# Optimization experiments

Measured on AMD Instinct MI355X. Metric: run time of the kernel, lower is better.

## Reference

```python
import jax, jax.numpy as jnp
import numpy as np

N_EMBD = 1024
N_HEAD = 16
B, T = 4, 2048

def setup_inputs() -> dict:
    key = jax.random.key(0)
    ks = jax.random.split(key, 5)
    s_attn = 1.0 / np.sqrt(N_EMBD)
    s_proj = 1.0 / np.sqrt(N_EMBD)
    return {
        "x": jax.random.normal(ks[0], (B, T, N_EMBD), dtype=jnp.float32),
        "w_attn": jax.random.uniform(ks[1], (N_EMBD, 3 * N_EMBD), jnp.float32, -s_attn, s_attn),
        "b_attn": jax.random.uniform(ks[2], (3 * N_EMBD,), jnp.float32, -s_attn, s_attn),
        "w_proj": jax.random.uniform(ks[3], (N_EMBD, N_EMBD), jnp.float32, -s_proj, s_proj),
        "b_proj": jax.random.uniform(ks[4], (N_EMBD,), jnp.float32, -s_proj, s_proj),
    }

def reference(x, w_attn, b_attn, w_proj, b_proj):
    Bx, Tx, C = x.shape
    hd = C // N_HEAD  # head dim
    qkv = x @ w_attn + b_attn                       # [B,T,3C]
    q, k, v = jnp.split(qkv, 3, axis=-1)
    # [B,T,C] -> [B,H,T,hd]
    def heads(t):
        return t.reshape(Bx, Tx, N_HEAD, hd).transpose(0, 2, 1, 3)
    q, k, v = heads(q), heads(k), heads(v)
    att = jnp.einsum('bhqd,bhkd->bhqk', q, k) * (1.0 / np.sqrt(hd))
    causal = jnp.tril(jnp.ones((Tx, Tx), dtype=bool))
    att = jnp.where(causal, att, -jnp.inf)
    att = jax.nn.softmax(att, axis=-1)
    y = jnp.einsum('bhqk,bhkd->bhqd', att, v)       # [B,H,T,hd]
    y = y.transpose(0, 2, 1, 3).reshape(Bx, Tx, C)
    return y @ w_proj + b_proj
```

## Files before the change

kernel.cpp:

```cpp
#include <hip/hip_runtime.h>
#include <cstdint>

typedef unsigned short u16;
typedef short s16x8 __attribute__((ext_vector_type(8)));
typedef short s16x4 __attribute__((ext_vector_type(4)));
typedef float f32x4 __attribute__((ext_vector_type(4)));

#define B_   4
#define T_   2048
#define C_   1024
#define H_   16
#define HD_  64
#define M_   8192
#define N3_  3072

#define QSCALE 0.18033688011112042f

__device__ inline u16 f2b(float f) {
  union { float f; uint32_t u; } v; v.f = f;
  uint32_t u = v.u;
  return (u16)((u + 0x7FFFu + ((u >> 16) & 1u)) >> 16);
}

__device__ inline f32x4 mfma16(s16x4 a, s16x4 b, f32x4 c) {
#if __has_builtin(__builtin_amdgcn_mfma_f32_16x16x16bf16_1k)
  return __builtin_amdgcn_mfma_f32_16x16x16bf16_1k(a, b, c, 0, 0, 0);
#else
  f32x4 d;
  asm("v_mfma_f32_16x16x16_bf16 %0, %1, %2, %3"
      : "=v"(d) : "v"(a), "v"(b), "v"(c));
  return d;
#endif
}

__device__ inline void gload_lds16(const void* g, void* l) {
  __builtin_amdgcn_global_load_lds(
      (const __attribute__((address_space(1))) void*)g,
      (__attribute__((address_space(3))) void*)l, 16, 0, 0);
}

__global__ __launch_bounds__(256) void cvt_f32_bf16(
    const float* __restrict__ in, u16* __restrict__ out, int n) {
  int i = (blockIdx.x * 256 + threadIdx.x) * 8;
  if (i >= n) return;
  float4 a = *(const float4*)(in + i);
  float4 b = *(const float4*)(in + i + 4);
  s16x8 r;
  r[0] = (short)f2b(a.x); r[1] = (short)f2b(a.y);
  r[2] = (short)f2b(a.z); r[3] = (short)f2b(a.w);
  r[4] = (short)f2b(b.x); r[5] = (short)f2b(b.y);
  r[6] = (short)f2b(b.z); r[7] = (short)f2b(b.w);
  *(s16x8*)(out + i) = r;
}

__global__ __launch_bounds__(256) void cvt_transpose(
    const float* __restrict__ W, u16* __restrict__ WT, int K, int N) {
  __shared__ u16 tile[64][65];
  int n0 = blockIdx.x * 64, k0 = blockIdx.y * 64;
  int j = threadIdx.x & 63, i0 = threadIdx.x >> 6;
#pragma unroll
  for (int i = i0; i < 64; i += 4)
    tile[i][j] = f2b(W[(size_t)(k0 + i) * N + n0 + j]);
  __syncthreads();
#pragma unroll
  for (int i = i0; i < 64; i += 4)
    WT[(size_t)(n0 + i) * K + k0 + j] = tile[j][i];
}

template <int MODE>
__global__ __launch_bounds__(256, 2) void gemm_bt(
    const u16* __restrict__ A, const u16* __restrict__ Bt,
    const float* __restrict__ bias, float* __restrict__ outf,
    u16* __restrict__ qo, u16* __restrict__ ko, u16* __restrict__ vo,
    int M, int N, int K) {
  __shared__ u16 As[128 * 32];
  __shared__ u16 Bs[128 * 32];
  int bid = blockIdx.x;
  int nbn = N >> 7;
  int bm = bid / nbn, bn = bid % nbn;
  int m0 = bm * 128, n0 = bn * 128;
  int tid = threadIdx.x;
  int lane = tid & 63, w = tid >> 6;
  int wm = (w >> 1) * 64, wn = (w & 1) * 64;
  int l15 = lane & 15, g = lane >> 4;

  f32x4 acc[4][4] = {};

  for (int kb = 0; kb < K; kb += 32) {
    __syncthreads();
#pragma unroll
    for (int it = 0; it < 2; ++it) {
      int idx = it * 256 + tid;
      int row = idx >> 2, kc = (idx & 3) * 8;
      gload_lds16(A  + (size_t)(m0 + row) * K + kb + kc, &As[idx * 8]);
      gload_lds16(Bt + (size_t)(n0 + row) * K + kb + kc, &Bs[idx * 8]);
    }
    __syncthreads();

    s16x8 af[4], bf[4];
#pragma unroll
    for (int mi = 0; mi < 4; ++mi)
      af[mi] = *(const s16x8*)&As[(wm + mi * 16 + l15) * 32 + g * 8];
#pragma unroll
    for (int ni = 0; ni < 4; ++ni)
      bf[ni] = *(const s16x8*)&Bs[(wn + ni * 16 + l15) * 32 + g * 8];
#pragma unroll
    for (int mi = 0; mi < 4; ++mi)
#pragma unroll
      for (int ni = 0; ni < 4; ++ni)
        acc[mi][ni] = __builtin_amdgcn_mfma_f32_16x16x32_bf16(
            af[mi], bf[ni], acc[mi][ni], 0, 0, 0);
  }

#pragma unroll
  for (int mi = 0; mi < 4; ++mi)
#pragma unroll
    for (int ni = 0; ni < 4; ++ni) {
      int col = n0 + wn + ni * 16 + l15;
      float bv = bias[col];
#pragma unroll
      for (int r = 0; r < 4; ++r) {
        int row = m0 + wm + mi * 16 + g * 4 + r;
        float val = acc[mi][ni][r] + bv;
        if (MODE == 0) {
          outf[(size_t)row * N + col] = val;
        } else {
          int which = col >> 10, hc = col & 1023;
          int h = hc >> 6, d = hc & 63;
          int b = row >> 11, t = row & 2047;
          if (which == 0) val *= QSCALE;
          u16* dst = (which == 0) ? qo : (which == 1) ? ko : vo;
          dst[(((size_t)(b * 16 + h)) * 2048 + t) * 64 + d] = f2b(val);
        }
      }
    }
}

__global__ __launch_bounds__(256, 2) void attn_fwd(
    const u16* __restrict__ Q, const u16* __restrict__ Kg,
    const u16* __restrict__ V, u16* __restrict__ Y) {
  __shared__ u16 Ks[64 * 72];
  __shared__ u16 Vt[64 * 66];

  int bid = blockIdx.x;
  int bh = bid & 63;
  int qt = 31 - (bid >> 6);
  int tid = threadIdx.x, lane = tid & 63, w = tid >> 6;
  int l15 = lane & 15, g = lane >> 4;

  const u16* Qh = Q  + (size_t)bh * T_ * HD_;
  const u16* Kh = Kg + (size_t)bh * T_ * HD_;
  const u16* Vh = V  + (size_t)bh * T_ * HD_;

  int q0 = qt * 64 + w * 16;
  int qrow = q0 + l15;

  s16x8 qa[2];
#pragma unroll
  for (int ks = 0; ks < 2; ++ks)
    qa[ks] = *(const s16x8*)(Qh + (size_t)qrow * HD_ + g * 8 + ks * 32);

  f32x4 oacc[4] = {};
  float m = -3.0e30f, l = 0.f;

  int vr = tid >> 3, vc = (tid & 7) * 8;
  int kr = tid >> 2, kc = (tid & 3) * 16;

  int ntile = qt + 1;
  for (int kt = 0; kt < ntile; ++kt) {
    int kvb = kt * 64;
    __syncthreads();
    {
      const u16* krow = Kh + (size_t)(kvb + kr) * HD_ + kc;
      *(s16x8*)&Ks[kr * 72 + kc]     = *(const s16x8*)krow;
      *(s16x8*)&Ks[kr * 72 + kc + 8] = *(const s16x8*)(krow + 8);
#pragma unroll
      for (int hh = 0; hh < 2; ++hh) {
        int kv = vr + hh * 32;
        s16x8 vv = *(const s16x8*)(Vh + (size_t)(kvb + kv) * HD_ + vc);
#pragma unroll
        for (int i = 0; i < 8; ++i) Vt[(vc + i) * 66 + kv] = (u16)vv[i];
      }
    }
    __syncthreads();

    f32x4 sacc[4] = {};
#pragma unroll
    for (int cf = 0; cf < 4; ++cf)
#pragma unroll
      for (int ks = 0; ks < 2; ++ks) {
        s16x8 kb = *(const s16x8*)&Ks[(cf * 16 + l15) * 72 + g * 8 + ks * 32];
        sacc[cf] = __builtin_amdgcn_mfma_f32_16x16x32_bf16(kb, qa[ks], sacc[cf], 0, 0, 0);
      }

    if (kt == qt) {
#pragma unroll
      for (int cf = 0; cf < 4; ++cf)
#pragma unroll
        for (int r = 0; r < 4; ++r) {
          int kv = kvb + cf * 16 + g * 4 + r;
          if (kv > qrow) sacc[cf][r] = -1e30f;
        }
    }

    float mx = sacc[0][0];
#pragma unroll
    for (int cf = 0; cf < 4; ++cf)
#pragma unroll
      for (int r = 0; r < 4; ++r) mx = fmaxf(mx, sacc[cf][r]);
    mx = fmaxf(mx, __shfl_xor(mx, 16, 64));
    mx = fmaxf(mx, __shfl_xor(mx, 32, 64));

    float mn = fmaxf(m, mx);
    float alpha = __builtin_amdgcn_exp2f(m - mn);
    m = mn;

    float rs = 0.f;
#pragma unroll
    for (int cf = 0; cf < 4; ++cf)
#pragma unroll
      for (int r = 0; r < 4; ++r) {
        float p = __builtin_amdgcn_exp2f(sacc[cf][r] - mn);
        sacc[cf][r] = p;
        rs += p;
      }
    rs += __shfl_xor(rs, 16, 64);
    rs += __shfl_xor(rs, 32, 64);
    l = l * alpha + rs;
#pragma unroll
    for (int df = 0; df < 4; ++df)
#pragma unroll
      for (int r = 0; r < 4; ++r) oacc[df][r] *= alpha;

#pragma unroll
    for (int cf = 0; cf < 4; ++cf) {
      s16x4 pb;
#pragma unroll
      for (int r = 0; r < 4; ++r) pb[r] = (short)f2b(sacc[cf][r]);
#pragma unroll
      for (int df = 0; df < 4; ++df) {
        const u16* vp = &Vt[(df * 16 + l15) * 66 + cf * 16 + g * 4];
        union { uint32_t u[2]; s16x4 s; } va;
        va.u[0] = *(const uint32_t*)(vp);
        va.u[1] = *(const uint32_t*)(vp + 2);
        oacc[df] = mfma16(va.s, pb, oacc[df]);
      }
    }
  }

  int b = bh >> 4, h = bh & 15;
  float inv = 1.0f / l;
  u16* yrow = Y + ((size_t)b * T_ + qrow) * C_ + h * 64;
#pragma unroll
  for (int df = 0; df < 4; ++df) {
    s16x4 o;
#pragma unroll
    for (int r = 0; r < 4; ++r) o[r] = (short)f2b(oacc[df][r] * inv);
    *(s16x4*)(yrow + df * 16 + g * 4) = o;
  }
}

extern "C" void kernel_launch(void* const* d_in, const int* in_sizes, int n_in,
                              void* d_out, int out_size, void* d_ws, size_t ws_size,
                              hipStream_t stream) {
  const float* x      = (const float*)d_in[0];
  const float* w_attn = (const float*)d_in[1];
  const float* b_attn = (const float*)d_in[2];
  const float* w_proj = (const float*)d_in[3];
  const float* b_proj = (const float*)d_in[4];
  float* out = (float*)d_out;

  u16* ws  = (u16*)d_ws;
  u16* xb  = ws;
  u16* wat = xb  + (size_t)M_ * C_;
  u16* wpt = wat + (size_t)N3_ * C_;
  u16* q   = wpt + (size_t)C_ * C_;
  u16* k   = q   + (size_t)M_ * C_;
  u16* v   = k   + (size_t)M_ * C_;
  u16* ya  = xb;

  cvt_f32_bf16<<<dim3((M_ * C_) / (256 * 8)), dim3(256), 0, stream>>>(x, xb, M_ * C_);
  cvt_transpose<<<dim3(N3_ / 64, C_ / 64), dim3(256), 0, stream>>>(w_attn, wat, C_, N3_);
  cvt_transpose<<<dim3(C_ / 64, C_ / 64), dim3(256), 0, stream>>>(w_proj, wpt, C_, C_);

  gemm_bt<1><<<dim3((M_ / 128) * (N3_ / 128)), dim3(256), 0, stream>>>(
      xb, wat, b_attn, nullptr, q, k, v, M_, N3_, C_);

  attn_fwd<<<dim3(64 * 32), dim3(256), 0, stream>>>(q, k, v, ya);

  gemm_bt<0><<<dim3((M_ / 128) * (C_ / 128)), dim3(256), 0, stream>>>(
      ya, wpt, b_proj, out, nullptr, nullptr, nullptr, M_, C_, C_);
}
```

Baseline: 200.4 us.

## Store V transposed from QKV GEMM, prefetch K/V tiles, swizzle LDS, lazy rescale

The QKV GEMM epilogue now writes V transposed ([bh][d][t]) with vectorized stores. Attention can then load V tiles directly instead of transposing them element by element in LDS. The attention kernel register-prefetches the next K/V tile during compute, uses XOR-swizzled unpadded LDS, and skips the softmax rescale unless the max grows by more than 8 (log2 units). The GEMM also remaps block IDs for L2 locality, and attention asks for occupancy 4. Risks include register pressure under the higher occupancy bound and the lazy-rescale threshold allowing larger intermediate exponents.

```diff
diff --git a/kernel.cpp b/kernel.cpp
--- a/kernel.cpp
+++ b/kernel.cpp
@@ -75,7 +75,9 @@
     int M, int N, int K) {
   __shared__ u16 As[128 * 32];
   __shared__ u16 Bs[128 * 32];
-  int bid = blockIdx.x;
+  int nwg = gridDim.x;
+  int bid0 = blockIdx.x;
+  int bid = (bid0 & 7) * (nwg >> 3) + (bid0 >> 3);
   int nbn = N >> 7;
   int bm = bid / nbn, bn = bid % nbn;
   int m0 = bm * 128, n0 = bn * 128;
@@ -118,29 +120,37 @@
     for (int ni = 0; ni < 4; ++ni) {
       int col = n0 + wn + ni * 16 + l15;
       float bv = bias[col];
-#pragma unroll
-      for (int r = 0; r < 4; ++r) {
-        int row = m0 + wm + mi * 16 + g * 4 + r;
-        float val = acc[mi][ni][r] + bv;
-        if (MODE == 0) {
-          outf[(size_t)row * N + col] = val;
+      int row0 = m0 + wm + mi * 16 + g * 4;
+      if (MODE == 0) {
+#pragma unroll
+        for (int r = 0; r < 4; ++r)
+          outf[(size_t)(row0 + r) * N + col] = acc[mi][ni][r] + bv;
+      } else {
+        int which = col >> 10, hc = col & 1023;
+        int h = hc >> 6, d = hc & 63;
+        int b = row0 >> 11, t0 = row0 & 2047;
+        if (which == 2) {
+          s16x4 pv;
+#pragma unroll
+          for (int r = 0; r < 4; ++r) pv[r] = (short)f2b(acc[mi][ni][r] + bv);
+          *(s16x4*)(vo + ((size_t)((b * 16 + h) * 64 + d)) * 2048 + t0) = pv;
         } else {
-          int which = col >> 10, hc = col & 1023;
-          int h = hc >> 6, d = hc & 63;
-          int b = row >> 11, t = row & 2047;
-          if (which == 0) val *= QSCALE;
-          u16* dst = (which == 0) ? qo : (which == 1) ? ko : vo;
-          dst[(((size_t)(b * 16 + h)) * 2048 + t) * 64 + d] = f2b(val);
+          u16* dst = (which == 0) ? qo : ko;
+          float sc2 = (which == 0) ? QSCALE : 1.0f;
+#pragma unroll
+          for (int r = 0; r < 4; ++r)
+            dst[(((size_t)(b * 16 + h)) * 2048 + (t0 + r)) * 64 + d] =
+                f2b((acc[mi][ni][r] + bv) * sc2);
         }
       }
     }
 }
 
-__global__ __launch_bounds__(256, 2) void attn_fwd(
+__global__ __launch_bounds__(256, 4) void attn_fwd(
     const u16* __restrict__ Q, const u16* __restrict__ Kg,
-    const u16* __restrict__ V, u16* __restrict__ Y) {
-  __shared__ u16 Ks[64 * 72];
-  __shared__ u16 Vt[64 * 66];
+    const u16* __restrict__ Vt, u16* __restrict__ Y) {
+  __shared__ u16 Ks[64 * 64];
+  __shared__ u16 Vs[64 * 64];
 
   int bid = blockIdx.x;
   int bh = bid & 63;
@@ -150,7 +160,7 @@
 
   const u16* Qh = Q  + (size_t)bh * T_ * HD_;
   const u16* Kh = Kg + (size_t)bh * T_ * HD_;
-  const u16* Vh = V  + (size_t)bh * T_ * HD_;
+  const u16* Vh = Vt + (size_t)bh * HD_ * T_;
 
   int q0 = qt * 64 + w * 16;
   int qrow = q0 + l15;
@@ -163,33 +173,42 @@
   f32x4 oacc[4] = {};
   float m = -3.0e30f, l = 0.f;
 
-  int vr = tid >> 3, vc = (tid & 7) * 8;
-  int kr = tid >> 2, kc = (tid & 3) * 16;
+  int sr = tid >> 3, sc = tid & 7;
+  int wswz = (sr & 7) << 4;
+  int rswz = (l15 & 7) << 4;
+  char* KsB = (char*)Ks;
+  char* VsB = (char*)Vs;
+
+  s16x8 kr0 = *(const s16x8*)(Kh + (size_t)sr * HD_ + sc * 8);
+  s16x8 kr1 = *(const s16x8*)(Kh + (size_t)(sr + 32) * HD_ + sc * 8);
+  s16x8 vr0 = *(const s16x8*)(Vh + (size_t)sr * T_ + sc * 8);
+  s16x8 vr1 = *(const s16x8*)(Vh + (size_t)(sr + 32) * T_ + sc * 8);
 
   int ntile = qt + 1;
   for (int kt = 0; kt < ntile; ++kt) {
     int kvb = kt * 64;
     __syncthreads();
+    *(s16x8*)(KsB + sr * 128 + ((sc * 16) ^ wswz))        = kr0;
+    *(s16x8*)(KsB + (sr + 32) * 128 + ((sc * 16) ^ wswz)) = kr1;
+    *(s16x8*)(VsB + sr * 128 + ((sc * 16) ^ wswz))        = vr0;
+    *(s16x8*)(VsB + (sr + 32) * 128 + ((sc * 16) ^ wswz)) = vr1;
+    __syncthreads();
+
     {
-      const u16* krow = Kh + (size_t)(kvb + kr) * HD_ + kc;
-      *(s16x8*)&Ks[kr * 72 + kc]     = *(const s16x8*)krow;
-      *(s16x8*)&Ks[kr * 72 + kc + 8] = *(const s16x8*)(krow + 8);
-#pragma unroll
-      for (int hh = 0; hh < 2; ++hh) {
-        int kv = vr + hh * 32;
-        s16x8 vv = *(const s16x8*)(Vh + (size_t)(kvb + kv) * HD_ + vc);
-#pragma unroll
-        for (int i = 0; i < 8; ++i) Vt[(vc + i) * 66 + kv] = (u16)vv[i];
-      }
-    }
-    __syncthreads();
+      int kvn = (kt + 1 < ntile) ? (kt + 1) * 64 : 0;
+      kr0 = *(const s16x8*)(Kh + (size_t)(kvn + sr) * HD_ + sc * 8);
+      kr1 = *(const s16x8*)(Kh + (size_t)(kvn + sr + 32) * HD_ + sc * 8);
+      vr0 = *(const s16x8*)(Vh + (size_t)sr * T_ + kvn + sc * 8);
+      vr1 = *(const s16x8*)(Vh + (size_t)(sr + 32) * T_ + kvn + sc * 8);
+    }
 
     f32x4 sacc[4] = {};
 #pragma unroll
     for (int cf = 0; cf < 4; ++cf)
 #pragma unroll
       for (int ks = 0; ks < 2; ++ks) {
-        s16x8 kb = *(const s16x8*)&Ks[(cf * 16 + l15) * 72 + g * 8 + ks * 32];
+        s16x8 kb = *(const s16x8*)(KsB + (cf * 16 + l15) * 128 +
+                                   ((g * 16 + ks * 64) ^ rswz));
         sacc[cf] = __builtin_amdgcn_mfma_f32_16x16x32_bf16(kb, qa[ks], sacc[cf], 0, 0, 0);
       }
 
@@ -203,34 +222,37 @@
         }
     }
 
-    float mx = sacc[0][0];
-#pragma unroll
-    for (int cf = 0; cf < 4; ++cf)
-#pragma unroll
-      for (int r = 0; r < 4; ++r) mx = fmaxf(mx, sacc[cf][r]);
+    float t0 = fmaxf(fmaxf(sacc[0][0], sacc[0][1]), fmaxf(sacc[0][2], sacc[0][3]));
+    float t1 = fmaxf(fmaxf(sacc[1][0], sacc[1][1]), fmaxf(sacc[1][2], sacc[1][3]));
+    float t2 = fmaxf(fmaxf(sacc[2][0], sacc[2][1]), fmaxf(sacc[2][2], sacc[2][3]));
+    float t3 = fmaxf(fmaxf(sacc[3][0], sacc[3][1]), fmaxf(sacc[3][2], sacc[3][3]));
+    float mx = fmaxf(fmaxf(t0, t1), fmaxf(t2, t3));
     mx = fmaxf(mx, __shfl_xor(mx, 16, 64));
     mx = fmaxf(mx, __shfl_xor(mx, 32, 64));
 
-    float mn = fmaxf(m, mx);
-    float alpha = __builtin_amdgcn_exp2f(m - mn);
-    m = mn;
+    if (!__all(mx <= m + 8.0f)) {
+      float mn = fmaxf(m, mx);
+      float alpha = __builtin_amdgcn_exp2f(m - mn);
+      m = mn;
+      l *= alpha;
+#pragma unroll
+      for (int df = 0; df < 4; ++df)
+#pragma unroll
+        for (int r = 0; r < 4; ++r) oacc[df][r] *= alpha;
+    }
 
     float rs = 0.f;
 #pragma unroll
     for (int cf = 0; cf < 4; ++cf)
 #pragma unroll
       for (int r = 0; r < 4; ++r) {
-        float p = __builtin_amdgcn_exp2f(sacc[cf][r] - mn);
+        float p = __builtin_amdgcn_exp2f(sacc[cf][r] - m);
         sacc[cf][r] = p;
         rs += p;
       }
     rs += __shfl_xor(rs, 16, 64);
     rs += __shfl_xor(rs, 32, 64);
-    l = l * alpha + rs;
-#pragma unroll
-    for (int df = 0; df < 4; ++df)
-#pragma unroll
-      for (int r = 0; r < 4; ++r) oacc[df][r] *= alpha;
+    l += rs;
 
 #pragma unroll
     for (int cf = 0; cf < 4; ++cf) {
@@ -239,11 +261,9 @@
       for (int r = 0; r < 4; ++r) pb[r] = (short)f2b(sacc[cf][r]);
 #pragma unroll
       for (int df = 0; df < 4; ++df) {
-        const u16* vp = &Vt[(df * 16 + l15) * 66 + cf * 16 + g * 4];
-        union { uint32_t u[2]; s16x4 s; } va;
-        va.u[0] = *(const uint32_t*)(vp);
-        va.u[1] = *(const uint32_t*)(vp + 2);
-        oacc[df] = mfma16(va.s, pb, oacc[df]);
+        s16x4 va = *(const s16x4*)(VsB + (df * 16 + l15) * 128 +
+                                   ((cf * 32 + g * 8) ^ rswz));
+        oacc[df] = mfma16(va, pb, oacc[df]);
       }
     }
   }
```

Result: faster. 187.0 us (-6.7%).
